# Kernel optimization log

Measured on AMD Instinct MI355X. Metric: run time of the kernel, lower is better.

## Reference

```python
import jax, jax.numpy as jnp
import numpy as np

B, S, D, DK, DV = 8, 2048, 256, 128, 128

def setup_inputs() -> dict:
    key = jax.random.key(0)
    ks = jax.random.split(key, 9)
    return {
        "x_q": jax.random.normal(ks[0], (B, S, D), jnp.float32),
        "x_k": jax.random.normal(ks[1], (B, S, D), jnp.float32),
        "x_v": jax.random.normal(ks[2], (B, S, D), jnp.float32),
        "Wq": jax.random.normal(ks[3], (D, DK), jnp.float32) * (1.0 / np.sqrt(D)),
        "bq": jax.random.normal(ks[4], (DK,), jnp.float32) * 0.02,
        "Wk": jax.random.normal(ks[5], (D, DK), jnp.float32) * (1.0 / np.sqrt(D)),
        "bk": jax.random.normal(ks[6], (DK,), jnp.float32) * 0.02,
        "Wv": jax.random.normal(ks[7], (D, DV), jnp.float32) * (1.0 / np.sqrt(D)),
        "bv": jax.random.normal(ks[8], (DV,), jnp.float32) * 0.02,
    }

def reference(x_q, x_k, x_v, Wq, bq, Wk, bk, Wv, bv):
    # Dense projections: [B,S,D] @ [D,dk] + bias
    q = jnp.einsum("bsd,dk->bsk", x_q, Wq) + bq
    k = jnp.einsum("bsd,dk->bsk", x_k, Wk) + bk
    v = jnp.einsum("bsd,dv->bsv", x_v, Wv) + bv
    scale = 1.0 / np.sqrt(Wq.shape[1]).astype(np.float32)  # 1/sqrt(d_k)
    scores = jnp.einsum("bqk,bsk->bqs", q, k) * scale       # [B,S,S]
    attn = jax.nn.softmax(scores, axis=-1)
    return jnp.einsum("bqs,bsv->bqv", attn, v)               # [B,S,d_v]
```

## Files before the change

### kernel.cpp

```cpp
#include <hip/hip_runtime.h>
#include <stdint.h>

typedef float    f32x4  __attribute__((ext_vector_type(4)));
typedef float    f32x16 __attribute__((ext_vector_type(16)));
typedef _Float16 f16x8  __attribute__((ext_vector_type(8)));
typedef _Float16 f16x4  __attribute__((ext_vector_type(4)));
typedef unsigned int u32x4 __attribute__((ext_vector_type(4)));

#define SPLIT 8
#define NTILES 8

__device__ __forceinline__ f32x4 mfma16(f16x8 a, f16x8 b, f32x4 c) {
    return __builtin_amdgcn_mfma_f32_16x16x32_f16(a, b, c, 0, 0, 0);
}
__device__ __forceinline__ f32x16 mfma32(f16x8 a, f16x8 b, f32x16 c) {
    return __builtin_amdgcn_mfma_f32_32x32x16_f16(a, b, c, 0, 0, 0);
}
__device__ __forceinline__ void gll16(const _Float16* g, _Float16* l) {
    __builtin_amdgcn_global_load_lds(
        (const __attribute__((address_space(1))) void*)g,
        (__attribute__((address_space(3))) void*)l, 16, 0, 0);
}

__global__ __launch_bounds__(256) void prep_weights(
    const float* __restrict__ Wq, const float* __restrict__ Wk,
    const float* __restrict__ Wv, _Float16* __restrict__ wt) {
    __shared__ float Ls[64 * 65];
    const int bx = blockIdx.x;
    const int w  = bx >> 3, t = bx & 7;
    const int k0 = (t >> 1) * 64, n0 = (t & 1) * 64;
    const float* W = (w == 0) ? Wq : (w == 1) ? Wk : Wv;
    const int tid = threadIdx.x;
    #pragma unroll
    for (int i = 0; i < 16; i++) {
        int idx = i * 256 + tid;
        int r = idx >> 6, c = idx & 63;
        Ls[r * 65 + c] = W[(k0 + r) * 128 + n0 + c];
    }
    __syncthreads();
    #pragma unroll
    for (int i = 0; i < 16; i++) {
        int idx = i * 256 + tid;
        int r2 = idx >> 6, c2 = idx & 63;
        wt[w * 32768 + (n0 + r2) * 256 + k0 + c2] = (_Float16)Ls[c2 * 65 + r2];
    }
}

__global__ __launch_bounds__(256) void proj_kernel(
    const float* __restrict__ xq, const float* __restrict__ xk,
    const float* __restrict__ xv, const _Float16* __restrict__ wt,
    const float* __restrict__ bq, const float* __restrict__ bk,
    const float* __restrict__ bv,
    _Float16* __restrict__ qo, _Float16* __restrict__ ko,
    _Float16* __restrict__ vtmp)
{
    const int mode = blockIdx.y;
    const float*    X    = mode == 0 ? xq : mode == 1 ? xk : xv;
    const float*    bias = mode == 0 ? bq : mode == 1 ? bk : bv;
    const _Float16* W    = wt + mode * 32768;
    _Float16*       Y    = mode == 0 ? qo : mode == 1 ? ko : vtmp;

    const int tid  = threadIdx.x;
    const int wave = tid >> 6, lane = tid & 63;
    const int ln   = lane & 15, qd = lane >> 4;
    const int row0 = blockIdx.x * 64 + wave * 16;

    const float*    xrow = X + (size_t)(row0 + ln) * 256 + qd * 8;
    const _Float16* wb   = W + ln * 256 + qd * 8;

    f32x4 acc[8];
    #pragma unroll
    for (int i = 0; i < 8; i++) acc[i] = (f32x4){0.f, 0.f, 0.f, 0.f};

    #pragma unroll
    for (int kk = 0; kk < 8; kk++) {
        f32x4 a0 = *(const f32x4*)(xrow + kk * 32);
        f32x4 a1 = *(const f32x4*)(xrow + kk * 32 + 4);
        f16x8 af;
        af[0] = (_Float16)a0[0]; af[1] = (_Float16)a0[1];
        af[2] = (_Float16)a0[2]; af[3] = (_Float16)a0[3];
        af[4] = (_Float16)a1[0]; af[5] = (_Float16)a1[1];
        af[6] = (_Float16)a1[2]; af[7] = (_Float16)a1[3];
        #pragma unroll
        for (int nt = 0; nt < 8; nt++) {
            f16x8 bf = *(const f16x8*)(wb + nt * 4096 + kk * 32);
            acc[nt] = mfma16(af, bf, acc[nt]);
        }
    }

    const float SC = 0.08838834764831845f * 1.4426950408889634f;
    #pragma unroll
    for (int nt = 0; nt < 8; nt++) {
        int col = nt * 16 + ln;
        float bb = bias[col];
        #pragma unroll
        for (int r = 0; r < 4; r++) {
            int orow = row0 + qd * 4 + r;
            float val = acc[nt][r] + bb;
            if (mode == 0) val *= SC;
            Y[(size_t)orow * 128 + col] = (_Float16)val;
        }
    }
}

__global__ __launch_bounds__(256) void transpose_v(
    const _Float16* __restrict__ vtmp, _Float16* __restrict__ vt)
{
    __shared__ __align__(16) _Float16 Ls[64 * 72];
    const int b  = blockIdx.z;
    const int s0 = blockIdx.x * 64;
    const int d0 = blockIdx.y * 64;
    const int tid = threadIdx.x;
    #pragma unroll
    for (int i = 0; i < 2; i++) {
        int idx = i * 256 + tid;
        int r = idx >> 3, c = (idx & 7) * 8;
        *(f16x8*)&Ls[r * 72 + c] =
            *(const f16x8*)(vtmp + (size_t)(b * 2048 + s0 + r) * 128 + d0 + c);
    }
    __syncthreads();
    #pragma unroll
    for (int i = 0; i < 2; i++) {
        int idx = i * 256 + tid;
        int dr = idx >> 3, sc8 = (idx & 7) * 8;
        f16x8 o;
        #pragma unroll
        for (int j = 0; j < 8; j++) o[j] = Ls[(sc8 + j) * 72 + dr];
        *(f16x8*)(vt + (size_t)(b * 128 + d0 + dr) * 2048 + s0 + sc8) = o;
    }
}

__global__ __launch_bounds__(256, 3) void attn_kernel(
    const _Float16* __restrict__ qp, const _Float16* __restrict__ kp,
    const _Float16* __restrict__ vtp, _Float16* __restrict__ opart,
    float2* __restrict__ ml)
{
    const int bid = blockIdx.x;
    const int gx  = bid & 7;
    const int q0i = (bid >> 3) & 15;
    const int gg  = bid >> 7;
    const int g   = gg * 8 + gx;
    const int b   = g >> 3;
    const int z   = g & 7;
    const int q0  = q0i * 128;

    const int tid  = threadIdx.x;
    const int wave = tid >> 6, lane = tid & 63;
    const int ln   = lane & 31, h = lane >> 5;

    __shared__ __align__(16) _Float16 smem[16896];

    const _Float16* qbase =
        qp + (size_t)(b * 2048 + q0 + wave * 32 + ln) * 128 + h * 8;
    f16x8 qf[8];
    #pragma unroll
    for (int kb = 0; kb < 8; kb++) qf[kb] = *(const f16x8*)(qbase + kb * 16);

    f32x16 o[4];
    #pragma unroll
    for (int i = 0; i < 4; i++) o[i] = (f32x16){};
    float m_run = -1e30f, l_run = 0.f;

    const _Float16* kbase = kp + (size_t)b * 2048 * 128;
    const _Float16* vbase = vtp + (size_t)b * 128 * 2048;
    const int kt0 = z * NTILES;

    auto stage = [&](int kt, int buf) {
        const _Float16* ks = kbase + (size_t)kt * 4096;
        const _Float16* vs = vbase + kt * 32;
        _Float16* kdst = smem + buf * 4096;
        _Float16* vdst = smem + 8192 + buf * 4096;
        #pragma unroll
        for (int j = 0; j < 2; j++) {
            int p  = wave * 128 + j * 64 + lane;
            int r  = p >> 4, c = p & 15;
            int cs = c ^ (r & 15);
            gll16(ks + r * 128 + cs * 8, kdst + (wave * 128 + j * 64) * 8);
            int rv = p >> 2, cv = p & 3;
            gll16(vs + (size_t)rv * 2048 + cv * 8, vdst + (wave * 128 + j * 64) * 8);
        }
    };

    stage(kt0, 0);

    for (int it = 0; it < NTILES; it++) {
        __syncthreads();
        if (it + 1 < NTILES) stage(kt0 + it + 1, (it + 1) & 1);
        const _Float16* kb_ = smem + (it & 1) * 4096;
        const _Float16* vb_ = smem + 8192 + (it & 1) * 4096;

        f32x16 sc = (f32x16){};
        #pragma unroll
        for (int kb = 0; kb < 8; kb++) {
            int phys = (kb * 2 + h) ^ (ln & 15);
            f16x8 kf = *(const f16x8*)&kb_[ln * 128 + phys * 8];
            sc = mfma32(kf, qf[kb], sc);
        }

        float t = sc[0];
        #pragma unroll
        for (int i = 1; i < 16; i++) t = fmaxf(t, sc[i]);
        t = fmaxf(t, __shfl_xor(t, 32));
        const float mnew  = fmaxf(m_run, t);
        const float alpha = exp2f(m_run - mnew);

        f16x4 phg[4];
        float ssum = 0.f;
        #pragma unroll
        for (int gi = 0; gi < 4; gi++) {
            #pragma unroll
            for (int e = 0; e < 4; e++) {
                float p = exp2f(sc[gi * 4 + e] - mnew);
                ssum += p;
                phg[gi][e] = (_Float16)p;
            }
        }
        ssum += __shfl_xor(ssum, 32);
        l_run = l_run * alpha + ssum;
        m_run = mnew;

        #pragma unroll
        for (int dvb = 0; dvb < 4; dvb++) o[dvb] *= alpha;

        #pragma unroll
        for (int kb2 = 0; kb2 < 2; kb2++) {
            f16x4 own0 = phg[2 * kb2], own1 = phg[2 * kb2 + 1];
            f16x4 send = h ? own0 : own1;
            unsigned long long sv = __builtin_bit_cast(unsigned long long, send);
            unsigned long long rv = __shfl_xor(sv, 32);
            f16x4 recv = __builtin_bit_cast(f16x4, rv);
            f16x4 lo = h ? recv : own0;
            f16x4 hi = h ? own1 : recv;
            f16x8 bf = __builtin_shufflevector(lo, hi, 0, 1, 2, 3, 4, 5, 6, 7);
            #pragma unroll
            for (int dvb = 0; dvb < 4; dvb++) {
                f16x8 vf = *(const f16x8*)&vb_[(dvb * 32 + ln) * 32 +
                                               (kb2 * 2 + h) * 8];
                o[dvb] = mfma32(vf, bf, o[dvb]);
            }
        }
    }

    __syncthreads();
    _Float16* pw = smem + wave * 4224;
    #pragma unroll
    for (int dvb = 0; dvb < 4; dvb++) {
        #pragma unroll
        for (int gi = 0; gi < 4; gi++) {
            f16x4 w4;
            #pragma unroll
            for (int e = 0; e < 4; e++) w4[e] = (_Float16)o[dvb][gi * 4 + e];
            *(f16x4*)&pw[ln * 132 + dvb * 32 + gi * 8 + h * 4] = w4;
        }
    }
    const size_t prow = (size_t)(z * 8 + b) * 2048 + q0 + wave * 32;
    __builtin_amdgcn_s_waitcnt(0);
    #pragma unroll
    for (int p = 0; p < 2; p++) {
        int q = p * 16 + (lane >> 2), part = lane & 3;
        #pragma unroll
        for (int i2 = 0; i2 < 4; i2++) {
            f16x8 v8 = *(const f16x8*)&pw[q * 132 + part * 8 + i2 * 32];
            *(f16x8*)(opart + (prow + q) * 128 + part * 8 + i2 * 32) = v8;
        }
    }
    if (lane < 32) {
        float2 v; v.x = m_run; v.y = l_run;
        ml[prow + ln] = v;
    }
}

__global__ __launch_bounds__(256) void merge_kernel(
    const _Float16* __restrict__ opart, const float2* __restrict__ ml,
    float* __restrict__ out)
{
    const int t = threadIdx.x;
    const int r = t >> 4, cg = t & 15;
    const size_t row = (size_t)blockIdx.x * 16 + r;

    float M = -1e30f;
    #pragma unroll
    for (int zi = 0; zi < SPLIT; zi++)
        M = fmaxf(M, ml[(size_t)zi * 16384 + row].x);
    float L = 0.f;
    float acc[8] = {0.f, 0.f, 0.f, 0.f, 0.f, 0.f, 0.f, 0.f};
    #pragma unroll
    for (int zi = 0; zi < SPLIT; zi++) {
        float2 p = ml[(size_t)zi * 16384 + row];
        float w = exp2f(p.x - M);
        L += w * p.y;
        f16x8 v = *(const f16x8*)&opart[((size_t)zi * 16384 + row) * 128 + cg * 8];
        #pragma unroll
        for (int j = 0; j < 8; j++) acc[j] += w * (float)v[j];
    }
    const float inv = 1.0f / L;
    float* op = out + row * 128 + cg * 8;
    f32x4 lo = (f32x4){acc[0] * inv, acc[1] * inv, acc[2] * inv, acc[3] * inv};
    f32x4 hi = (f32x4){acc[4] * inv, acc[5] * inv, acc[6] * inv, acc[7] * inv};
    *(f32x4*)op = lo;
    *(f32x4*)(op + 4) = hi;
}

extern "C" void kernel_launch(void* const* d_in, const int* in_sizes, int n_in,
                              void* d_out, int out_size, void* d_ws, size_t ws_size,
                              hipStream_t stream) {
    const float* xq = (const float*)d_in[0];
    const float* xk = (const float*)d_in[1];
    const float* xv = (const float*)d_in[2];
    const float* Wq = (const float*)d_in[3];
    const float* bq = (const float*)d_in[4];
    const float* Wk = (const float*)d_in[5];
    const float* bk = (const float*)d_in[6];
    const float* Wv = (const float*)d_in[7];
    const float* bv = (const float*)d_in[8];
    float* out = (float*)d_out;

    char* ws = (char*)d_ws;
    _Float16* wt    = (_Float16*)ws;
    _Float16* qo    = (_Float16*)(ws + 196608);
    _Float16* ko    = (_Float16*)(ws + 196608 + 4194304);
    _Float16* vt    = (_Float16*)(ws + 196608 + 2 * 4194304);
    float2*   ml    = (float2*)  (ws + 196608 + 3 * 4194304);
    _Float16* opart = (_Float16*)(ws + 196608 + 3 * 4194304 + 1048576);
    _Float16* vtmp  = opart;

    hipLaunchKernelGGL(prep_weights, dim3(24), dim3(256), 0, stream,
                       Wq, Wk, Wv, wt);
    hipLaunchKernelGGL(proj_kernel, dim3(256, 3), dim3(256), 0, stream,
                       xq, xk, xv, wt, bq, bk, bv, qo, ko, vtmp);
    hipLaunchKernelGGL(transpose_v, dim3(32, 2, 8), dim3(256), 0, stream,
                       vtmp, vt);
    hipLaunchKernelGGL(attn_kernel, dim3(16 * 8 * SPLIT), dim3(256), 0, stream,
                       qo, ko, vt, opart, ml);
    hipLaunchKernelGGL(merge_kernel, dim3(1024), dim3(256), 0, stream,
                       opart, ml, out);
}
```

Before: 167.4 us.

## Fuse V transpose into projection, halve split-K, unroll attention tile loop

Result: faster. 161.8 us (-3.4%).

```diff
diff --git a/kernel.cpp b/kernel.cpp
--- a/kernel.cpp
+++ b/kernel.cpp
@@ -7,8 +7,8 @@
 typedef _Float16 f16x4  __attribute__((ext_vector_type(4)));
 typedef unsigned int u32x4 __attribute__((ext_vector_type(4)));
 
-#define SPLIT 8
-#define NTILES 8
+#define SPLIT 4
+#define NTILES 16
 
 __device__ __forceinline__ f32x4 mfma16(f16x8 a, f16x8 b, f32x4 c) {
     return __builtin_amdgcn_mfma_f32_16x16x32_f16(a, b, c, 0, 0, 0);
@@ -52,13 +52,14 @@
     const float* __restrict__ bq, const float* __restrict__ bk,
     const float* __restrict__ bv,
     _Float16* __restrict__ qo, _Float16* __restrict__ ko,
-    _Float16* __restrict__ vtmp)
+    _Float16* __restrict__ vt)
 {
     const int mode = blockIdx.y;
     const float*    X    = mode == 0 ? xq : mode == 1 ? xk : xv;
     const float*    bias = mode == 0 ? bq : mode == 1 ? bk : bv;
     const _Float16* W    = wt + mode * 32768;
-    _Float16*       Y    = mode == 0 ? qo : mode == 1 ? ko : vtmp;
+
+    __shared__ __align__(16) _Float16 Ls[128 * 66];
 
     const int tid  = threadIdx.x;
     const int wave = tid >> 6, lane = tid & 63;
@@ -89,44 +90,41 @@
     }
 
     const float SC = 0.08838834764831845f * 1.4426950408889634f;
-    #pragma unroll
-    for (int nt = 0; nt < 8; nt++) {
-        int col = nt * 16 + ln;
-        float bb = bias[col];
-        #pragma unroll
-        for (int r = 0; r < 4; r++) {
-            int orow = row0 + qd * 4 + r;
-            float val = acc[nt][r] + bb;
-            if (mode == 0) val *= SC;
-            Y[(size_t)orow * 128 + col] = (_Float16)val;
-        }
-    }
-}
-
-__global__ __launch_bounds__(256) void transpose_v(
-    const _Float16* __restrict__ vtmp, _Float16* __restrict__ vt)
-{
-    __shared__ __align__(16) _Float16 Ls[64 * 72];
-    const int b  = blockIdx.z;
-    const int s0 = blockIdx.x * 64;
-    const int d0 = blockIdx.y * 64;
-    const int tid = threadIdx.x;
-    #pragma unroll
-    for (int i = 0; i < 2; i++) {
-        int idx = i * 256 + tid;
-        int r = idx >> 3, c = (idx & 7) * 8;
-        *(f16x8*)&Ls[r * 72 + c] =
-            *(const f16x8*)(vtmp + (size_t)(b * 2048 + s0 + r) * 128 + d0 + c);
-    }
-    __syncthreads();
-    #pragma unroll
-    for (int i = 0; i < 2; i++) {
-        int idx = i * 256 + tid;
-        int dr = idx >> 3, sc8 = (idx & 7) * 8;
-        f16x8 o;
-        #pragma unroll
-        for (int j = 0; j < 8; j++) o[j] = Ls[(sc8 + j) * 72 + dr];
-        *(f16x8*)(vt + (size_t)(b * 128 + d0 + dr) * 2048 + s0 + sc8) = o;
+    if (mode != 2) {
+        _Float16* Y = mode == 0 ? qo : ko;
+        #pragma unroll
+        for (int nt = 0; nt < 8; nt++) {
+            int col = nt * 16 + ln;
+            float bb = bias[col];
+            #pragma unroll
+            for (int r = 0; r < 4; r++) {
+                int orow = row0 + qd * 4 + r;
+                float val = acc[nt][r] + bb;
+                if (mode == 0) val *= SC;
+                Y[(size_t)orow * 128 + col] = (_Float16)val;
+            }
+        }
+    } else {
+        #pragma unroll
+        for (int nt = 0; nt < 8; nt++) {
+            int col = nt * 16 + ln;
+            float bb = bias[col];
+            #pragma unroll
+            for (int r = 0; r < 4; r++) {
+                int srow = wave * 16 + qd * 4 + r;
+                Ls[col * 66 + srow] = (_Float16)(acc[nt][r] + bb);
+            }
+        }
+        __syncthreads();
+        const int bb2 = row0 >> 11;
+        const int s0  = (blockIdx.x * 64) & 2047;
+        #pragma unroll
+        for (int i = 0; i < 4; i++) {
+            int g  = i * 256 + tid;
+            int dv = g >> 3, off = (g & 7) * 8;
+            f16x8 v8 = *(const f16x8*)&Ls[dv * 66 + off];
+            *(f16x8*)(vt + ((size_t)(bb2 * 128 + dv)) * 2048 + s0 + off) = v8;
+        }
     }
 }
 
@@ -140,8 +138,8 @@
     const int q0i = (bid >> 3) & 15;
     const int gg  = bid >> 7;
     const int g   = gg * 8 + gx;
-    const int b   = g >> 3;
-    const int z   = g & 7;
+    const int b   = g >> 2;
+    const int z   = g & 3;
     const int q0  = q0i * 128;
 
     const int tid  = threadIdx.x;
@@ -149,6 +147,25 @@
     const int ln   = lane & 31, h = lane >> 5;
 
     __shared__ __align__(16) _Float16 smem[16896];
+
+    int koff[8], voff[2][4];
+    #pragma unroll
+    for (int kb = 0; kb < 8; kb++)
+        koff[kb] = ln * 128 + (((kb * 2 + h) ^ (ln & 15)) * 8);
+    #pragma unroll
+    for (int kb2 = 0; kb2 < 2; kb2++)
+        #pragma unroll
+        for (int dvb = 0; dvb < 4; dvb++)
+            voff[kb2][dvb] = 8192 + (dvb * 32 + ln) * 32 + (kb2 * 2 + h) * 8;
+    int kidx[2], vidx[2], dst[2];
+    #pragma unroll
+    for (int j = 0; j < 2; j++) {
+        int p = wave * 128 + j * 64 + lane;
+        int r = p >> 4, c = p & 15;
+        kidx[j] = r * 128 + ((c ^ (r & 15)) * 8);
+        vidx[j] = (p >> 2) * 2048 + (p & 3) * 8;
+        dst[j]  = (wave * 128 + j * 64) * 8;
+    }
 
     const _Float16* qbase =
         qp + (size_t)(b * 2048 + q0 + wave * 32 + ln) * 128 + h * 8;
@@ -172,31 +189,19 @@
         _Float16* vdst = smem + 8192 + buf * 4096;
         #pragma unroll
         for (int j = 0; j < 2; j++) {
-            int p  = wave * 128 + j * 64 + lane;
-            int r  = p >> 4, c = p & 15;
-            int cs = c ^ (r & 15);
-            gll16(ks + r * 128 + cs * 8, kdst + (wave * 128 + j * 64) * 8);
-            int rv = p >> 2, cv = p & 3;
-            gll16(vs + (size_t)rv * 2048 + cv * 8, vdst + (wave * 128 + j * 64) * 8);
+            gll16(ks + kidx[j], kdst + dst[j]);
+            gll16(vs + vidx[j], vdst + dst[j]);
         }
     };
 
-    stage(kt0, 0);
-
-    for (int it = 0; it < NTILES; it++) {
-        __syncthreads();
-        if (it + 1 < NTILES) stage(kt0 + it + 1, (it + 1) & 1);
-        const _Float16* kb_ = smem + (it & 1) * 4096;
-        const _Float16* vb_ = smem + 8192 + (it & 1) * 4096;
-
+    auto do_tile = [&](const int BUF) {
+        const int KO = BUF * 4096, VO = BUF * 4096;
         f32x16 sc = (f32x16){};
         #pragma unroll
         for (int kb = 0; kb < 8; kb++) {
-            int phys = (kb * 2 + h) ^ (ln & 15);
-            f16x8 kf = *(const f16x8*)&kb_[ln * 128 + phys * 8];
+            f16x8 kf = *(const f16x8*)&smem[KO + koff[kb]];
             sc = mfma32(kf, qf[kb], sc);
         }
-
         float t = sc[0];
         #pragma unroll
         for (int i = 1; i < 16; i++) t = fmaxf(t, sc[i]);
@@ -219,8 +224,10 @@
         l_run = l_run * alpha + ssum;
         m_run = mnew;
 
-        #pragma unroll
-        for (int dvb = 0; dvb < 4; dvb++) o[dvb] *= alpha;
+        if (__any(alpha < 1.0f)) {
+            #pragma unroll
+            for (int dvb = 0; dvb < 4; dvb++) o[dvb] *= alpha;
+        }
 
         #pragma unroll
         for (int kb2 = 0; kb2 < 2; kb2++) {
@@ -234,11 +241,21 @@
             f16x8 bf = __builtin_shufflevector(lo, hi, 0, 1, 2, 3, 4, 5, 6, 7);
             #pragma unroll
             for (int dvb = 0; dvb < 4; dvb++) {
-                f16x8 vf = *(const f16x8*)&vb_[(dvb * 32 + ln) * 32 +
-                                               (kb2 * 2 + h) * 8];
+                f16x8 vf = *(const f16x8*)&smem[VO + voff[kb2][dvb]];
                 o[dvb] = mfma32(vf, bf, o[dvb]);
             }
         }
+    };
+
+    stage(kt0, 0);
+    #pragma unroll 1
+    for (int ht = 0; ht < NTILES / 2; ht++) {
+        __syncthreads();
+        if (2 * ht + 1 < NTILES) stage(kt0 + 2 * ht + 1, 1);
+        do_tile(0);
+        __syncthreads();
+        if (2 * ht + 2 < NTILES) stage(kt0 + 2 * ht + 2, 0);
+        do_tile(1);
     }
 
     __syncthreads();
@@ -322,14 +339,11 @@
     _Float16* vt    = (_Float16*)(ws + 196608 + 2 * 4194304);
     float2*   ml    = (float2*)  (ws + 196608 + 3 * 4194304);
     _Float16* opart = (_Float16*)(ws + 196608 + 3 * 4194304 + 1048576);
-    _Float16* vtmp  = opart;
 
     hipLaunchKernelGGL(prep_weights, dim3(24), dim3(256), 0, stream,
                        Wq, Wk, Wv, wt);
     hipLaunchKernelGGL(proj_kernel, dim3(256, 3), dim3(256), 0, stream,
-                       xq, xk, xv, wt, bq, bk, bv, qo, ko, vtmp);
-    hipLaunchKernelGGL(transpose_v, dim3(32, 2, 8), dim3(256), 0, stream,
-                       vtmp, vt);
+                       xq, xk, xv, wt, bq, bk, bv, qo, ko, vt);
     hipLaunchKernelGGL(attn_kernel, dim3(16 * 8 * SPLIT), dim3(256), 0, stream,
                        qo, ko, vt, opart, ml);
     hipLaunchKernelGGL(merge_kernel, dim3(1024), dim3(256), 0, stream,
```
